# Performance work log

Hardware: AMD Instinct MI355X
Metric: run time of the kernel (lower is better)

Reference implementation:

```python
import jax, jax.numpy as jnp
import numpy as np

EPS = 1e-5  # nn.LayerNorm default

def _conv1x1(x, W):
    # x: (B,C,H,W), W: (O,C) -> (B,O,H,W)
    return jnp.einsum('bchw,oc->bohw', x, W)

def setup_inputs() -> dict:
    key = jax.random.key(0)
    kx, k1, k2, k3, k4, k5 = jax.random.split(key, 6)
    B, C, H, W = 16, 512, 64, 64
    inner = C // 2
    s = 1.0 / np.sqrt(C)
    return {
        'x':   jax.random.normal(kx, (B, C, H, W), dtype=jnp.float32),
        'Wsq': jax.random.normal(k1, (inner, C), dtype=jnp.float32) * s,
        'Wsv': jax.random.normal(k2, (inner, C), dtype=jnp.float32) * s,
        'Wcq': jax.random.normal(k3, (1, C), dtype=jnp.float32) * s,
        'Wcv': jax.random.normal(k4, (inner, C), dtype=jnp.float32) * s,
        'Wcz': jax.random.normal(k5, (C, inner), dtype=jnp.float32) * (1.0 / np.sqrt(inner)),
        'gamma': jnp.ones((C,), dtype=jnp.float32),
        'beta':  jnp.zeros((C,), dtype=jnp.float32),
    }

def _channel_pool(x, Wcq, Wcv, Wcz, gamma, beta):
    B, C, H, W = x.shape
    HW = H * W
    # channel_q: 1x1 conv to 1 channel -> (B, HW), softmax over HW
    cm = jnp.einsum('bchw,c->bhw', x, Wcq[0]).reshape(B, HW)
    cm = jax.nn.softmax(cm, axis=-1)                      # (B, HW)
    # channel_v: (B, inner, HW)
    iv = _conv1x1(x, Wcv).reshape(B, Wcv.shape[0], HW)
    context = jnp.einsum('bkn,bn->bk', iv, cm)            # (B, inner)
    z = jnp.einsum('bk,ok->bo', context, Wcz)             # (B, out)
    mu = jnp.mean(z, axis=-1, keepdims=True)
    var = jnp.mean((z - mu) ** 2, axis=-1, keepdims=True)
    zn = (z - mu) * jax.lax.rsqrt(var + EPS) * gamma + beta
    mask = jax.nn.sigmoid(zn)[:, :, None, None]           # (B, out, 1, 1)
    return x * mask

def _spatial_pool(x, Wsq, Wsv):
    B, C, H, W = x.shape
    HW = H * W
    g = _conv1x1(x, Wsq)                                  # (B, inner, H, W)
    avg = jnp.mean(g, axis=(2, 3))                        # (B, inner)
    avg = jax.nn.softmax(avg, axis=-1)                    # softmax over inner channels
    theta = _conv1x1(x, Wsv).reshape(B, Wsv.shape[0], HW) # (B, inner, HW)
    ctx = jnp.einsum('bk,bkn->bn', avg, theta).reshape(B, 1, H, W)
    return x * jax.nn.sigmoid(ctx)

def reference(x, Wsq, Wsv, Wcq, Wcv, Wcz, gamma, beta):
    # layout='parallel'
    ch = _channel_pool(x, Wcq, Wcv, Wcz, gamma, beta)
    sp = _spatial_pool(x, Wsq, Wsv)
    return ch + sp
```

## Files before the change

kernel.cpp:

```cpp
#include <hip/hip_runtime.h>
#include <math.h>

#define BB 16
#define CC 512
#define HWN 4096
#define INNER 256
#define EPSV 1e-5f

__device__ __forceinline__ float wave_sum(float s) {
    for (int off = 32; off; off >>= 1) s += __shfl_down(s, off);
    return s;
}
__device__ __forceinline__ float block_sum(float v, volatile float* s_red) {
    for (int off = 32; off; off >>= 1) v += __shfl_down(v, off);
    __syncthreads();
    if ((threadIdx.x & 63) == 0) s_red[threadIdx.x >> 6] = v;
    __syncthreads();
    return s_red[0] + s_red[1] + s_red[2] + s_red[3];
}
__device__ __forceinline__ float block_max(float v, volatile float* s_red) {
    for (int off = 32; off; off >>= 1) v = fmaxf(v, __shfl_down(v, off));
    __syncthreads();
    if ((threadIdx.x & 63) == 0) s_red[threadIdx.x >> 6] = v;
    __syncthreads();
    return fmaxf(fmaxf(s_red[0], s_red[1]), fmaxf(s_red[2], s_red[3]));
}
__device__ __forceinline__ float fsigmoid(float v) {
    return __builtin_amdgcn_rcpf(1.f + __expf(-v));
}

__global__ __launch_bounds__(256) void kA(
    const float* __restrict__ x, const float* __restrict__ wcq,
    float* __restrict__ cm_part, float* __restrict__ xsum_part)
{
    const int t = threadIdx.x, lane = t & 63, w = t >> 6;
    const int hw0 = blockIdx.x * 256;
    const int q   = blockIdx.y;
    const int c0  = q * 128;
    const int b   = blockIdx.z;
    __shared__ float s_w[128];
    __shared__ float s_cm[4][256];
    if (t < 128) s_w[t] = wcq[c0 + t];
    __syncthreads();
    const float* xb = x + ((size_t)b * CC + c0) * HWN + hw0 + lane * 4;
    float* xsp = xsum_part + ((size_t)b * 16 + blockIdx.x) * CC + c0;
    float4 acc = {0.f, 0.f, 0.f, 0.f};
    #pragma unroll 8
    for (int ci = 0; ci < 32; ++ci) {
        const int cl = w + ci * 4;
        float4 v = *(const float4*)(xb + (size_t)cl * HWN);
        const float wc = s_w[cl];
        acc.x = fmaf(v.x, wc, acc.x); acc.y = fmaf(v.y, wc, acc.y);
        acc.z = fmaf(v.z, wc, acc.z); acc.w = fmaf(v.w, wc, acc.w);
        float s = (v.x + v.y) + (v.z + v.w);
        s = wave_sum(s);
        if (lane == 0) xsp[cl] = s;
    }
    *(float4*)&s_cm[w][lane * 4] = acc;
    __syncthreads();
    cm_part[((size_t)b * 4 + q) * HWN + hw0 + t] =
        (s_cm[0][t] + s_cm[1][t]) + (s_cm[2][t] + s_cm[3][t]);
}

__global__ __launch_bounds__(256) void k2a_cmstats(
    const float* __restrict__ cm_part, float* __restrict__ cmstats)
{
    const int b = blockIdx.x, t = threadIdx.x;
    __shared__ float s_red[4];
    const float* p0 = cm_part + (size_t)b * 4 * HWN;
    const float* p1 = p0 + HWN;
    const float* p2 = p1 + HWN;
    const float* p3 = p2 + HWN;
    float lmax = -1e30f;
    #pragma unroll 4
    for (int i = t; i < HWN; i += 256)
        lmax = fmaxf(lmax, (p0[i] + p1[i]) + (p2[i] + p3[i]));
    lmax = block_max(lmax, s_red);
    float lsum = 0.f;
    #pragma unroll 4
    for (int i = t; i < HWN; i += 256)
        lsum += __expf((p0[i] + p1[i]) + (p2[i] + p3[i]) - lmax);
    lsum = block_sum(lsum, s_red);
    if (t == 0) {
        cmstats[2 * b]     = lmax;
        cmstats[2 * b + 1] = __builtin_amdgcn_rcpf(lsum);
    }
}

__global__ __launch_bounds__(256) void k_mvp(
    const float* __restrict__ W, const float* __restrict__ vpart,
    float* __restrict__ y, float scale)
{
    const int b = blockIdx.x, t = threadIdx.x, lane = t & 63, w = t >> 6;
    const int k0 = blockIdx.y * 64;
    __shared__ float s_v[CC];
    const float* xp = vpart + (size_t)b * 16 * CC;
    float a0 = 0.f, a1 = 0.f;
    #pragma unroll
    for (int blk = 0; blk < 16; ++blk) {
        a0 += xp[blk * CC + t];
        a1 += xp[blk * CC + t + 256];
    }
    s_v[t] = a0; s_v[t + 256] = a1;
    __syncthreads();
    float4 x0 = *(const float4*)&s_v[lane * 4];
    float4 x1 = *(const float4*)&s_v[256 + lane * 4];
    #pragma unroll 8
    for (int i = 0; i < 16; ++i) {
        const int k = k0 + w * 16 + i;
        const float* row = W + (size_t)k * CC + lane * 4;
        float4 q0 = *(const float4*)(row);
        float4 q1 = *(const float4*)(row + 256);
        float s = fmaf(q0.x,x0.x, fmaf(q0.y,x0.y, fmaf(q0.z,x0.z, q0.w*x0.w)))
                + fmaf(q1.x,x1.x, fmaf(q1.y,x1.y, fmaf(q1.z,x1.z, q1.w*x1.w)));
        s = wave_sum(s);
        if (lane == 0) y[b * INNER + k] = s * scale;
    }
}

__global__ __launch_bounds__(256) void k2c_wsv(
    const float* __restrict__ Wsv, const float* __restrict__ avg_logits,
    float* __restrict__ wsv_eff)
{
    const int b = blockIdx.x, t = threadIdx.x;
    const int c = blockIdx.y * 256 + t;
    __shared__ float s_red[4];
    __shared__ float s_sm[INNER];
    float a = avg_logits[b * INNER + t];
    float m = block_max(a, s_red);
    float e = __expf(a - m);
    float s2 = block_sum(e, s_red);
    s_sm[t] = e * __builtin_amdgcn_rcpf(s2);
    __syncthreads();
    float acc = 0.f;
    #pragma unroll 8
    for (int k = 0; k < INNER; ++k)
        acc = fmaf(s_sm[k], Wsv[(size_t)k * CC + c], acc);
    wsv_eff[b * CC + c] = acc;
}

__global__ __launch_bounds__(256) void kC(
    const float* __restrict__ x, const float* __restrict__ wsv_eff,
    const float* __restrict__ cm_part, const float* __restrict__ cmstats,
    float* __restrict__ ctx_part, float* __restrict__ xw_part)
{
    const int t = threadIdx.x, lane = t & 63, w = t >> 6;
    const int hw0 = blockIdx.x * 256;
    const int q   = blockIdx.y;
    const int c0  = q * 128;
    const int b   = blockIdx.z;
    __shared__ float s_w[128];
    __shared__ float s_m[256];
    __shared__ float s_cm[4][256];
    if (t < 128) s_w[t] = wsv_eff[b * CC + c0 + t];
    const float cmax = cmstats[2 * b], crinv = cmstats[2 * b + 1];
    const size_t cb = (size_t)b * 4 * HWN + hw0 + t;
    const float cmv = (cm_part[cb] + cm_part[cb + HWN])
                    + (cm_part[cb + 2 * HWN] + cm_part[cb + 3 * HWN]);
    s_m[t] = __expf(cmv - cmax) * crinv;
    __syncthreads();
    float4 mreg = *(const float4*)&s_m[lane * 4];
    const float* xb = x + ((size_t)b * CC + c0) * HWN + hw0 + lane * 4;
    float* xwp = xw_part + ((size_t)b * 16 + blockIdx.x) * CC + c0;
    float4 acc = {0.f, 0.f, 0.f, 0.f};
    #pragma unroll 8
    for (int ci = 0; ci < 32; ++ci) {
        const int cl = w + ci * 4;
        float4 v = *(const float4*)(xb + (size_t)cl * HWN);
        const float wc = s_w[cl];
        acc.x = fmaf(v.x, wc, acc.x); acc.y = fmaf(v.y, wc, acc.y);
        acc.z = fmaf(v.z, wc, acc.z); acc.w = fmaf(v.w, wc, acc.w);
        float s = fmaf(v.x,mreg.x, fmaf(v.y,mreg.y, fmaf(v.z,mreg.z, v.w*mreg.w)));
        s = wave_sum(s);
        if (lane == 0) xwp[cl] = s;
    }
    *(float4*)&s_cm[w][lane * 4] = acc;
    __syncthreads();
    ctx_part[((size_t)b * 4 + q) * HWN + hw0 + t] =
        (s_cm[0][t] + s_cm[1][t]) + (s_cm[2][t] + s_cm[3][t]);
}

__global__ __launch_bounds__(256) void k4b_z(
    const float* __restrict__ Wcz, const float* __restrict__ context,
    float* __restrict__ zbuf)
{
    const int b = blockIdx.x, t = threadIdx.x, lane = t & 63, w = t >> 6;
    const int o0 = blockIdx.y * 128;
    __shared__ float s_c[INNER];
    if (t < INNER) s_c[t] = context[b * INNER + t];
    __syncthreads();
    float4 cv = *(const float4*)&s_c[lane * 4];
    #pragma unroll 8
    for (int i = 0; i < 32; ++i) {
        const int o = o0 + w * 32 + i;
        float4 qv = *(const float4*)(Wcz + (size_t)o * INNER + lane * 4);
        float s = fmaf(qv.x,cv.x, fmaf(qv.y,cv.y, fmaf(qv.z,cv.z, qv.w*cv.w)));
        s = wave_sum(s);
        if (lane == 0) zbuf[b * CC + o] = s;
    }
}

__global__ __launch_bounds__(256) void k4c_ln(
    const float* __restrict__ gamma, const float* __restrict__ beta,
    const float* __restrict__ zbuf, float* __restrict__ maskbuf)
{
    const int b = blockIdx.x, t = threadIdx.x;
    __shared__ float s_red[4];
    float z0 = zbuf[b * CC + t], z1 = zbuf[b * CC + t + 256];
    float mu = block_sum(z0 + z1, s_red) * (1.f / CC);
    float d0 = z0 - mu, d1 = z1 - mu;
    float var = block_sum(d0 * d0 + d1 * d1, s_red) * (1.f / CC);
    float rstd = rsqrtf(var + EPSV);
    maskbuf[b * CC + t]       = fsigmoid(fmaf(d0 * rstd, gamma[t],       beta[t]));
    maskbuf[b * CC + t + 256] = fsigmoid(fmaf(d1 * rstd, gamma[t + 256], beta[t + 256]));
}

__global__ __launch_bounds__(256) void kE(
    const float* __restrict__ x, const float* __restrict__ ctx_part,
    const float* __restrict__ maskbuf, float* __restrict__ out)
{
    const int t  = threadIdx.x;
    const int hw = blockIdx.x * 1024 + t * 4;
    const int c0 = blockIdx.y * 16;
    const int b  = blockIdx.z;
    const size_t pb = (size_t)b * 4 * HWN + hw;
    float4 p0 = *(const float4*)(ctx_part + pb);
    float4 p1 = *(const float4*)(ctx_part + pb + HWN);
    float4 p2 = *(const float4*)(ctx_part + pb + 2 * HWN);
    float4 p3 = *(const float4*)(ctx_part + pb + 3 * HWN);
    float4 sg;
    sg.x = fsigmoid((p0.x + p1.x) + (p2.x + p3.x));
    sg.y = fsigmoid((p0.y + p1.y) + (p2.y + p3.y));
    sg.z = fsigmoid((p0.z + p1.z) + (p2.z + p3.z));
    sg.w = fsigmoid((p0.w + p1.w) + (p2.w + p3.w));
    const float* mb = maskbuf + b * CC + c0;
    const size_t base = ((size_t)b * CC + c0) * HWN + hw;
    #pragma unroll 4
    for (int ci = 0; ci < 16; ++ci) {
        const float m = mb[ci];
        float4 xv = *(const float4*)(x + base + (size_t)ci * HWN);
        float4 o;
        o.x = xv.x * (m + sg.x);
        o.y = xv.y * (m + sg.y);
        o.z = xv.z * (m + sg.z);
        o.w = xv.w * (m + sg.w);
        *(float4*)(out + base + (size_t)ci * HWN) = o;
    }
}

extern "C" void kernel_launch(void* const* d_in, const int* in_sizes, int n_in,
                              void* d_out, int out_size, void* d_ws, size_t ws_size,
                              hipStream_t stream) {
    const float* x     = (const float*)d_in[0];
    const float* Wsq   = (const float*)d_in[1];
    const float* Wsv   = (const float*)d_in[2];
    const float* Wcq   = (const float*)d_in[3];
    const float* Wcv   = (const float*)d_in[4];
    const float* Wcz   = (const float*)d_in[5];
    const float* gamma = (const float*)d_in[6];
    const float* beta  = (const float*)d_in[7];
    float* out = (float*)d_out;
    float* ws  = (float*)d_ws;

    float* cm_part    = ws;
    float* xsum_part  = ws + 262144;
    float* ctx_part   = ws + 393216;
    float* cmstats    = ws + 655360;
    float* wsv_eff    = ws + 655392;
    float* avg_logits = ws + 663584;
    float* context    = ws + 667680;
    float* zbuf       = ws + 671776;
    float* maskbuf    = ws + 679968;

    kA<<<dim3(16, 4, BB), 256, 0, stream>>>(x, Wcq, cm_part, xsum_part);
    k2a_cmstats<<<BB, 256, 0, stream>>>(cm_part, cmstats);
    k_mvp<<<dim3(BB, 4), 256, 0, stream>>>(Wsq, xsum_part, avg_logits, 1.0f / HWN);
    k2c_wsv<<<dim3(BB, 2), 256, 0, stream>>>(Wsv, avg_logits, wsv_eff);
    kC<<<dim3(16, 4, BB), 256, 0, stream>>>(x, wsv_eff, cm_part, cmstats, ctx_part, xsum_part);
    k_mvp<<<dim3(BB, 4), 256, 0, stream>>>(Wcv, xsum_part, context, 1.0f);
    k4b_z<<<dim3(BB, 4), 256, 0, stream>>>(Wcz, context, zbuf);
    k4c_ln<<<BB, 256, 0, stream>>>(gamma, beta, zbuf, maskbuf);
    kE<<<dim3(4, 32, BB), 256, 0, stream>>>(x, ctx_part, maskbuf, out);
}
```

Before: 381.4 us.

## Widen HW tiles in streaming passes, use LDS partial reductions, fuse small kernels

The two x-streaming kernels (kA, kC) now process 512 spatial positions per block with two float4 loads per thread, halving the grid. Per-channel sums go to a shared-memory tile and are reduced afterward instead of a wave shuffle reduction per channel. The softmax-stats and Wsq matvec kernels are merged into one launch via a blockIdx.y branch, and the Wcz matvec plus LayerNorm/sigmoid are fused into one 512-thread kernel, cutting the launch count from nine to seven. The trade-off is fewer blocks for latency hiding, more LDS per block (about 43 KB), and a serial 256-long dot product per thread in kD2.

```diff
diff --git a/kernel.cpp b/kernel.cpp
--- a/kernel.cpp
+++ b/kernel.cpp
@@ -25,6 +25,14 @@
     __syncthreads();
     return fmaxf(fmaxf(s_red[0], s_red[1]), fmaxf(s_red[2], s_red[3]));
 }
+__device__ __forceinline__ float block_sum8(float v, volatile float* s_red) {
+    for (int off = 32; off; off >>= 1) v += __shfl_down(v, off);
+    __syncthreads();
+    if ((threadIdx.x & 63) == 0) s_red[threadIdx.x >> 6] = v;
+    __syncthreads();
+    return ((s_red[0] + s_red[1]) + (s_red[2] + s_red[3]))
+         + ((s_red[4] + s_red[5]) + (s_red[6] + s_red[7]));
+}
 __device__ __forceinline__ float fsigmoid(float v) {
     return __builtin_amdgcn_rcpf(1.f + __expf(-v));
 }
@@ -34,87 +42,100 @@
     float* __restrict__ cm_part, float* __restrict__ xsum_part)
 {
     const int t = threadIdx.x, lane = t & 63, w = t >> 6;
-    const int hw0 = blockIdx.x * 256;
+    const int hw0 = blockIdx.x * 512;
     const int q   = blockIdx.y;
     const int c0  = q * 128;
     const int b   = blockIdx.z;
     __shared__ float s_w[128];
-    __shared__ float s_cm[4][256];
+    __shared__ float s_cm[4][512];
+    __shared__ float s_part[4][32][65];
     if (t < 128) s_w[t] = wcq[c0 + t];
     __syncthreads();
-    const float* xb = x + ((size_t)b * CC + c0) * HWN + hw0 + lane * 4;
-    float* xsp = xsum_part + ((size_t)b * 16 + blockIdx.x) * CC + c0;
-    float4 acc = {0.f, 0.f, 0.f, 0.f};
-    #pragma unroll 8
+    const float* xb = x + ((size_t)b * CC + c0) * HWN + hw0 + lane * 8;
+    float4 a0 = {0,0,0,0}, a1 = a0;
+    #pragma unroll 4
     for (int ci = 0; ci < 32; ++ci) {
         const int cl = w + ci * 4;
-        float4 v = *(const float4*)(xb + (size_t)cl * HWN);
+        const float* p = xb + (size_t)cl * HWN;
+        float4 v0 = *(const float4*)(p);
+        float4 v1 = *(const float4*)(p + 4);
         const float wc = s_w[cl];
-        acc.x = fmaf(v.x, wc, acc.x); acc.y = fmaf(v.y, wc, acc.y);
-        acc.z = fmaf(v.z, wc, acc.z); acc.w = fmaf(v.w, wc, acc.w);
-        float s = (v.x + v.y) + (v.z + v.w);
-        s = wave_sum(s);
-        if (lane == 0) xsp[cl] = s;
-    }
-    *(float4*)&s_cm[w][lane * 4] = acc;
-    __syncthreads();
-    cm_part[((size_t)b * 4 + q) * HWN + hw0 + t] =
-        (s_cm[0][t] + s_cm[1][t]) + (s_cm[2][t] + s_cm[3][t]);
-}
-
-__global__ __launch_bounds__(256) void k2a_cmstats(
-    const float* __restrict__ cm_part, float* __restrict__ cmstats)
-{
-    const int b = blockIdx.x, t = threadIdx.x;
+        a0.x = fmaf(v0.x, wc, a0.x); a0.y = fmaf(v0.y, wc, a0.y);
+        a0.z = fmaf(v0.z, wc, a0.z); a0.w = fmaf(v0.w, wc, a0.w);
+        a1.x = fmaf(v1.x, wc, a1.x); a1.y = fmaf(v1.y, wc, a1.y);
+        a1.z = fmaf(v1.z, wc, a1.z); a1.w = fmaf(v1.w, wc, a1.w);
+        s_part[w][ci][lane] = ((v0.x + v0.y) + (v0.z + v0.w))
+                            + ((v1.x + v1.y) + (v1.z + v1.w));
+    }
+    {
+        const int r = lane & 31;
+        const int j0 = (lane >> 5) * 32;
+        float xs = 0.f;
+        #pragma unroll
+        for (int j = 0; j < 32; ++j) xs += s_part[w][r][j0 + j];
+        xs += __shfl_down(xs, 32);
+        if (lane < 32)
+            xsum_part[((size_t)b * 8 + blockIdx.x) * CC + c0 + w + r * 4] = xs;
+    }
+    *(float4*)&s_cm[w][lane * 8]     = a0;
+    *(float4*)&s_cm[w][lane * 8 + 4] = a1;
+    __syncthreads();
+    float* cp = cm_part + ((size_t)b * 4 + q) * HWN + hw0;
+    cp[t]       = (s_cm[0][t]       + s_cm[1][t])       + (s_cm[2][t]       + s_cm[3][t]);
+    cp[t + 256] = (s_cm[0][t + 256] + s_cm[1][t + 256]) + (s_cm[2][t + 256] + s_cm[3][t + 256]);
+}
+
+__global__ __launch_bounds__(256) void kB1(
+    const float* __restrict__ Wsq, const float* __restrict__ cm_part,
+    const float* __restrict__ xsum_part,
+    float* __restrict__ cmstats, float* __restrict__ avg_logits)
+{
+    const int b = blockIdx.x, t = threadIdx.x, lane = t & 63, w = t >> 6;
     __shared__ float s_red[4];
-    const float* p0 = cm_part + (size_t)b * 4 * HWN;
-    const float* p1 = p0 + HWN;
-    const float* p2 = p1 + HWN;
-    const float* p3 = p2 + HWN;
-    float lmax = -1e30f;
-    #pragma unroll 4
-    for (int i = t; i < HWN; i += 256)
-        lmax = fmaxf(lmax, (p0[i] + p1[i]) + (p2[i] + p3[i]));
-    lmax = block_max(lmax, s_red);
-    float lsum = 0.f;
-    #pragma unroll 4
-    for (int i = t; i < HWN; i += 256)
-        lsum += __expf((p0[i] + p1[i]) + (p2[i] + p3[i]) - lmax);
-    lsum = block_sum(lsum, s_red);
-    if (t == 0) {
-        cmstats[2 * b]     = lmax;
-        cmstats[2 * b + 1] = __builtin_amdgcn_rcpf(lsum);
-    }
-}
-
-__global__ __launch_bounds__(256) void k_mvp(
-    const float* __restrict__ W, const float* __restrict__ vpart,
-    float* __restrict__ y, float scale)
-{
-    const int b = blockIdx.x, t = threadIdx.x, lane = t & 63, w = t >> 6;
-    const int k0 = blockIdx.y * 64;
     __shared__ float s_v[CC];
-    const float* xp = vpart + (size_t)b * 16 * CC;
-    float a0 = 0.f, a1 = 0.f;
-    #pragma unroll
-    for (int blk = 0; blk < 16; ++blk) {
-        a0 += xp[blk * CC + t];
-        a1 += xp[blk * CC + t + 256];
-    }
-    s_v[t] = a0; s_v[t + 256] = a1;
-    __syncthreads();
-    float4 x0 = *(const float4*)&s_v[lane * 4];
-    float4 x1 = *(const float4*)&s_v[256 + lane * 4];
-    #pragma unroll 8
-    for (int i = 0; i < 16; ++i) {
-        const int k = k0 + w * 16 + i;
-        const float* row = W + (size_t)k * CC + lane * 4;
-        float4 q0 = *(const float4*)(row);
-        float4 q1 = *(const float4*)(row + 256);
-        float s = fmaf(q0.x,x0.x, fmaf(q0.y,x0.y, fmaf(q0.z,x0.z, q0.w*x0.w)))
-                + fmaf(q1.x,x1.x, fmaf(q1.y,x1.y, fmaf(q1.z,x1.z, q1.w*x1.w)));
-        s = wave_sum(s);
-        if (lane == 0) y[b * INNER + k] = s * scale;
+    if (blockIdx.y == 4) {
+        const float* p0 = cm_part + (size_t)b * 4 * HWN;
+        const float* p1 = p0 + HWN;
+        const float* p2 = p1 + HWN;
+        const float* p3 = p2 + HWN;
+        float lmax = -1e30f;
+        #pragma unroll 4
+        for (int i = t; i < HWN; i += 256)
+            lmax = fmaxf(lmax, (p0[i] + p1[i]) + (p2[i] + p3[i]));
+        lmax = block_max(lmax, s_red);
+        float lsum = 0.f;
+        #pragma unroll 4
+        for (int i = t; i < HWN; i += 256)
+            lsum += __expf((p0[i] + p1[i]) + (p2[i] + p3[i]) - lmax);
+        lsum = block_sum(lsum, s_red);
+        if (t == 0) {
+            cmstats[2 * b]     = lmax;
+            cmstats[2 * b + 1] = __builtin_amdgcn_rcpf(lsum);
+        }
+    } else {
+        const int k0 = blockIdx.y * 64;
+        const float* xp = xsum_part + (size_t)b * 8 * CC;
+        float a0 = 0.f, a1 = 0.f;
+        #pragma unroll
+        for (int blk = 0; blk < 8; ++blk) {
+            a0 += xp[blk * CC + t];
+            a1 += xp[blk * CC + t + 256];
+        }
+        s_v[t] = a0; s_v[t + 256] = a1;
+        __syncthreads();
+        float4 x0 = *(const float4*)&s_v[lane * 4];
+        float4 x1 = *(const float4*)&s_v[256 + lane * 4];
+        #pragma unroll 8
+        for (int i = 0; i < 16; ++i) {
+            const int k = k0 + w * 16 + i;
+            const float* row = Wsq + (size_t)k * CC + lane * 4;
+            float4 q0 = *(const float4*)(row);
+            float4 q1 = *(const float4*)(row + 256);
+            float s = fmaf(q0.x,x0.x, fmaf(q0.y,x0.y, fmaf(q0.z,x0.z, q0.w*x0.w)))
+                    + fmaf(q1.x,x1.x, fmaf(q1.y,x1.y, fmaf(q1.z,x1.z, q1.w*x1.w)));
+            s = wave_sum(s);
+            if (lane == 0) avg_logits[b * INNER + k] = s * (1.0f / HWN);
+        }
     }
 }
 
@@ -145,74 +166,113 @@
     float* __restrict__ ctx_part, float* __restrict__ xw_part)
 {
     const int t = threadIdx.x, lane = t & 63, w = t >> 6;
-    const int hw0 = blockIdx.x * 256;
+    const int hw0 = blockIdx.x * 512;
     const int q   = blockIdx.y;
     const int c0  = q * 128;
     const int b   = blockIdx.z;
     __shared__ float s_w[128];
-    __shared__ float s_m[256];
-    __shared__ float s_cm[4][256];
+    __shared__ float s_m[512];
+    __shared__ float s_cm[4][512];
+    __shared__ float s_part[4][32][65];
     if (t < 128) s_w[t] = wsv_eff[b * CC + c0 + t];
     const float cmax = cmstats[2 * b], crinv = cmstats[2 * b + 1];
-    const size_t cb = (size_t)b * 4 * HWN + hw0 + t;
-    const float cmv = (cm_part[cb] + cm_part[cb + HWN])
-                    + (cm_part[cb + 2 * HWN] + cm_part[cb + 3 * HWN]);
-    s_m[t] = __expf(cmv - cmax) * crinv;
-    __syncthreads();
-    float4 mreg = *(const float4*)&s_m[lane * 4];
-    const float* xb = x + ((size_t)b * CC + c0) * HWN + hw0 + lane * 4;
-    float* xwp = xw_part + ((size_t)b * 16 + blockIdx.x) * CC + c0;
-    float4 acc = {0.f, 0.f, 0.f, 0.f};
-    #pragma unroll 8
+    {
+        const size_t cb = (size_t)b * 4 * HWN + hw0;
+        float cmv0 = (cm_part[cb + t]           + cm_part[cb + HWN + t])
+                   + (cm_part[cb + 2*HWN + t]   + cm_part[cb + 3*HWN + t]);
+        float cmv1 = (cm_part[cb + t+256]         + cm_part[cb + HWN + t+256])
+                   + (cm_part[cb + 2*HWN + t+256] + cm_part[cb + 3*HWN + t+256]);
+        s_m[t]       = __expf(cmv0 - cmax) * crinv;
+        s_m[t + 256] = __expf(cmv1 - cmax) * crinv;
+    }
+    __syncthreads();
+    float4 m0 = *(const float4*)&s_m[lane * 8];
+    float4 m1 = *(const float4*)&s_m[lane * 8 + 4];
+    const float* xb = x + ((size_t)b * CC + c0) * HWN + hw0 + lane * 8;
+    float4 a0 = {0,0,0,0}, a1 = a0;
+    #pragma unroll 4
     for (int ci = 0; ci < 32; ++ci) {
         const int cl = w + ci * 4;
-        float4 v = *(const float4*)(xb + (size_t)cl * HWN);
+        const float* p = xb + (size_t)cl * HWN;
+        float4 v0 = *(const float4*)(p);
+        float4 v1 = *(const float4*)(p + 4);
         const float wc = s_w[cl];
-        acc.x = fmaf(v.x, wc, acc.x); acc.y = fmaf(v.y, wc, acc.y);
-        acc.z = fmaf(v.z, wc, acc.z); acc.w = fmaf(v.w, wc, acc.w);
-        float s = fmaf(v.x,mreg.x, fmaf(v.y,mreg.y, fmaf(v.z,mreg.z, v.w*mreg.w)));
+        a0.x = fmaf(v0.x, wc, a0.x); a0.y = fmaf(v0.y, wc, a0.y);
+        a0.z = fmaf(v0.z, wc, a0.z); a0.w = fmaf(v0.w, wc, a0.w);
+        a1.x = fmaf(v1.x, wc, a1.x); a1.y = fmaf(v1.y, wc, a1.y);
+        a1.z = fmaf(v1.z, wc, a1.z); a1.w = fmaf(v1.w, wc, a1.w);
+        s_part[w][ci][lane] =
+              fmaf(v0.x,m0.x, fmaf(v0.y,m0.y, fmaf(v0.z,m0.z, v0.w*m0.w)))
+            + fmaf(v1.x,m1.x, fmaf(v1.y,m1.y, fmaf(v1.z,m1.z, v1.w*m1.w)));
+    }
+    {
+        const int r = lane & 31;
+        const int j0 = (lane >> 5) * 32;
+        float xs = 0.f;
+        #pragma unroll
+        for (int j = 0; j < 32; ++j) xs += s_part[w][r][j0 + j];
+        xs += __shfl_down(xs, 32);
+        if (lane < 32)
+            xw_part[((size_t)b * 8 + blockIdx.x) * CC + c0 + w + r * 4] = xs;
+    }
+    *(float4*)&s_cm[w][lane * 8]     = a0;
+    *(float4*)&s_cm[w][lane * 8 + 4] = a1;
+    __syncthreads();
+    float* cp = ctx_part + ((size_t)b * 4 + q) * HWN + hw0;
+    cp[t]       = (s_cm[0][t]       + s_cm[1][t])       + (s_cm[2][t]       + s_cm[3][t]);
+    cp[t + 256] = (s_cm[0][t + 256] + s_cm[1][t + 256]) + (s_cm[2][t + 256] + s_cm[3][t + 256]);
+}
+
+__global__ __launch_bounds__(256) void kD1(
+    const float* __restrict__ Wcv, const float* __restrict__ xw_part,
+    float* __restrict__ context)
+{
+    const int b = blockIdx.x, t = threadIdx.x, lane = t & 63, w = t >> 6;
+    const int k0 = blockIdx.y * 64;
+    __shared__ float s_v[CC];
+    const float* xp = xw_part + (size_t)b * 8 * CC;
+    float a0 = 0.f, a1 = 0.f;
+    #pragma unroll
+    for (int blk = 0; blk < 8; ++blk) {
+        a0 += xp[blk * CC + t];
+        a1 += xp[blk * CC + t + 256];
+    }
+    s_v[t] = a0; s_v[t + 256] = a1;
+    __syncthreads();
+    float4 x0 = *(const float4*)&s_v[lane * 4];
+    float4 x1 = *(const float4*)&s_v[256 + lane * 4];
+    #pragma unroll 8
+    for (int i = 0; i < 16; ++i) {
+        const int k = k0 + w * 16 + i;
+        const float* row = Wcv + (size_t)k * CC + lane * 4;
+        float4 q0 = *(const float4*)(row);
+        float4 q1 = *(const float4*)(row + 256);
+        float s = fmaf(q0.x,x0.x, fmaf(q0.y,x0.y, fmaf(q0.z,x0.z, q0.w*x0.w)))
+                + fmaf(q1.x,x1.x, fmaf(q1.y,x1.y, fmaf(q1.z,x1.z, q1.w*x1.w)));
         s = wave_sum(s);
-        if (lane == 0) xwp[cl] = s;
-    }
-    *(float4*)&s_cm[w][lane * 4] = acc;
-    __syncthreads();
-    ctx_part[((size_t)b * 4 + q) * HWN + hw0 + t] =
-        (s_cm[0][t] + s_cm[1][t]) + (s_cm[2][t] + s_cm[3][t]);
-}
-
-__global__ __launch_bounds__(256) void k4b_z(
+        if (lane == 0) context[b * INNER + k] = s;
+    }
+}
+
+__global__ __launch_bounds__(512) void kD2(
     const float* __restrict__ Wcz, const float* __restrict__ context,
-    float* __restrict__ zbuf)
-{
-    const int b = blockIdx.x, t = threadIdx.x, lane = t & 63, w = t >> 6;
-    const int o0 = blockIdx.y * 128;
+    const float* __restrict__ gamma, const float* __restrict__ beta,
+    float* __restrict__ maskbuf)
+{
+    const int b = blockIdx.x, t = threadIdx.x;
+    __shared__ float s_red[8];
     __shared__ float s_c[INNER];
     if (t < INNER) s_c[t] = context[b * INNER + t];
     __syncthreads();
-    float4 cv = *(const float4*)&s_c[lane * 4];
+    float acc = 0.f;
+    const float* wr = Wcz + (size_t)t * INNER;
     #pragma unroll 8
-    for (int i = 0; i < 32; ++i) {
-        const int o = o0 + w * 32 + i;
-        float4 qv = *(const float4*)(Wcz + (size_t)o * INNER + lane * 4);
-        float s = fmaf(qv.x,cv.x, fmaf(qv.y,cv.y, fmaf(qv.z,cv.z, qv.w*cv.w)));
-        s = wave_sum(s);
-        if (lane == 0) zbuf[b * CC + o] = s;
-    }
-}
-
-__global__ __launch_bounds__(256) void k4c_ln(
-    const float* __restrict__ gamma, const float* __restrict__ beta,
-    const float* __restrict__ zbuf, float* __restrict__ maskbuf)
-{
-    const int b = blockIdx.x, t = threadIdx.x;
-    __shared__ float s_red[4];
-    float z0 = zbuf[b * CC + t], z1 = zbuf[b * CC + t + 256];
-    float mu = block_sum(z0 + z1, s_red) * (1.f / CC);
-    float d0 = z0 - mu, d1 = z1 - mu;
-    float var = block_sum(d0 * d0 + d1 * d1, s_red) * (1.f / CC);
+    for (int k = 0; k < INNER; ++k) acc = fmaf(wr[k], s_c[k], acc);
+    float mu = block_sum8(acc, s_red) * (1.f / CC);
+    float d = acc - mu;
+    float var = block_sum8(d * d, s_red) * (1.f / CC);
     float rstd = rsqrtf(var + EPSV);
-    maskbuf[b * CC + t]       = fsigmoid(fmaf(d0 * rstd, gamma[t],       beta[t]));
-    maskbuf[b * CC + t + 256] = fsigmoid(fmaf(d1 * rstd, gamma[t + 256], beta[t + 256]));
+    maskbuf[b * CC + t] = fsigmoid(fmaf(d * rstd, gamma[t], beta[t]));
 }
 
 __global__ __launch_bounds__(256) void kE(
@@ -264,21 +324,18 @@
 
     float* cm_part    = ws;
     float* xsum_part  = ws + 262144;
-    float* ctx_part   = ws + 393216;
-    float* cmstats    = ws + 655360;
-    float* wsv_eff    = ws + 655392;
-    float* avg_logits = ws + 663584;
-    float* context    = ws + 667680;
-    float* zbuf       = ws + 671776;
-    float* maskbuf    = ws + 679968;
-
-    kA<<<dim3(16, 4, BB), 256, 0, stream>>>(x, Wcq, cm_part, xsum_part);
-    k2a_cmstats<<<BB, 256, 0, stream>>>(cm_part, cmstats);
-    k_mvp<<<dim3(BB, 4), 256, 0, stream>>>(Wsq, xsum_part, avg_logits, 1.0f / HWN);
+    float* ctx_part   = ws + 327680;
+    float* cmstats    = ws + 589824;
+    float* wsv_eff    = ws + 589856;
+    float* avg_logits = ws + 598048;
+    float* context    = ws + 602144;
+    float* maskbuf    = ws + 606240;
+
+    kA<<<dim3(8, 4, BB), 256, 0, stream>>>(x, Wcq, cm_part, xsum_part);
+    kB1<<<dim3(BB, 5), 256, 0, stream>>>(Wsq, cm_part, xsum_part, cmstats, avg_logits);
     k2c_wsv<<<dim3(BB, 2), 256, 0, stream>>>(Wsv, avg_logits, wsv_eff);
-    kC<<<dim3(16, 4, BB), 256, 0, stream>>>(x, wsv_eff, cm_part, cmstats, ctx_part, xsum_part);
-    k_mvp<<<dim3(BB, 4), 256, 0, stream>>>(Wcv, xsum_part, context, 1.0f);
-    k4b_z<<<dim3(BB, 4), 256, 0, stream>>>(Wcz, context, zbuf);
-    k4c_ln<<<BB, 256, 0, stream>>>(gamma, beta, zbuf, maskbuf);
+    kC<<<dim3(8, 4, BB), 256, 0, stream>>>(x, wsv_eff, cm_part, cmstats, ctx_part, xsum_part);
+    kD1<<<dim3(BB, 4), 256, 0, stream>>>(Wcv, xsum_part, context);
+    kD2<<<BB, 512, 0, stream>>>(Wcz, context, gamma, beta, maskbuf);
     kE<<<dim3(4, 32, BB), 256, 0, stream>>>(x, ctx_part, maskbuf, out);
 }
```

Measured after the change: 359.8 us. 5.7% less time.

## Fuse small GEMV/softmax/LN kernels and replace per-channel wave reductions with LDS transposes

Applied to the files above, without the earlier changes.

Merges the cmstats, Wsq matvec, softmax and Wsv projection into one kernel. It also merges the Wcv matvec, Wcz matvec, LayerNorm and the spatial sigmoid precompute into another, cutting the launch count from nine to five. In the x-streaming kernels, the per-iteration 64-lane shuffle reductions are replaced by writes to a padded LDS buffer, followed by one transposed reduction pass. The trade-off is fewer launches and less shuffle work against per-thread serial dot products over weight rows with strided, uncoalesced global reads, low-parallelism fused blocks, and extra LDS that may reduce occupancy.

```diff
diff --git a/kernel.cpp b/kernel.cpp
--- a/kernel.cpp
+++ b/kernel.cpp
@@ -24,6 +24,14 @@
     if ((threadIdx.x & 63) == 0) s_red[threadIdx.x >> 6] = v;
     __syncthreads();
     return fmaxf(fmaxf(s_red[0], s_red[1]), fmaxf(s_red[2], s_red[3]));
+}
+__device__ __forceinline__ float block_sum8(float v, volatile float* s_red) {
+    for (int off = 32; off; off >>= 1) v += __shfl_down(v, off);
+    __syncthreads();
+    if ((threadIdx.x & 63) == 0) s_red[threadIdx.x >> 6] = v;
+    __syncthreads();
+    return ((s_red[0] + s_red[1]) + (s_red[2] + s_red[3]))
+         + ((s_red[4] + s_red[5]) + (s_red[6] + s_red[7]));
 }
 __device__ __forceinline__ float fsigmoid(float v) {
     return __builtin_amdgcn_rcpf(1.f + __expf(-v));
@@ -40,11 +48,11 @@
     const int b   = blockIdx.z;
     __shared__ float s_w[128];
     __shared__ float s_cm[4][256];
+    __shared__ float s_part[4][32][65];
     if (t < 128) s_w[t] = wcq[c0 + t];
     __syncthreads();
     const float* xb = x + ((size_t)b * CC + c0) * HWN + hw0 + lane * 4;
-    float* xsp = xsum_part + ((size_t)b * 16 + blockIdx.x) * CC + c0;
-    float4 acc = {0.f, 0.f, 0.f, 0.f};
+    float4 acc = {0,0,0,0};
     #pragma unroll 8
     for (int ci = 0; ci < 32; ++ci) {
         const int cl = w + ci * 4;
@@ -52,9 +60,17 @@
         const float wc = s_w[cl];
         acc.x = fmaf(v.x, wc, acc.x); acc.y = fmaf(v.y, wc, acc.y);
         acc.z = fmaf(v.z, wc, acc.z); acc.w = fmaf(v.w, wc, acc.w);
-        float s = (v.x + v.y) + (v.z + v.w);
-        s = wave_sum(s);
-        if (lane == 0) xsp[cl] = s;
+        s_part[w][ci][lane] = (v.x + v.y) + (v.z + v.w);
+    }
+    {
+        const int r  = lane & 31;
+        const int j0 = (lane >> 5) * 32;
+        float xs = 0.f;
+        #pragma unroll
+        for (int j = 0; j < 32; ++j) xs += s_part[w][r][j0 + j];
+        xs += __shfl_down(xs, 32);
+        if (lane < 32)
+            xsum_part[((size_t)b * 16 + blockIdx.x) * CC + c0 + w + r * 4] = xs;
     }
     *(float4*)&s_cm[w][lane * 4] = acc;
     __syncthreads();
@@ -62,81 +78,68 @@
         (s_cm[0][t] + s_cm[1][t]) + (s_cm[2][t] + s_cm[3][t]);
 }
 
-__global__ __launch_bounds__(256) void k2a_cmstats(
-    const float* __restrict__ cm_part, float* __restrict__ cmstats)
+__global__ __launch_bounds__(256) void kBf(
+    const float* __restrict__ Wsq, const float* __restrict__ Wsv,
+    const float* __restrict__ cm_part, const float* __restrict__ xsum_part,
+    float* __restrict__ cmstats, float* __restrict__ wsv_eff)
 {
     const int b = blockIdx.x, t = threadIdx.x;
     __shared__ float s_red[4];
-    const float* p0 = cm_part + (size_t)b * 4 * HWN;
-    const float* p1 = p0 + HWN;
-    const float* p2 = p1 + HWN;
-    const float* p3 = p2 + HWN;
-    float lmax = -1e30f;
-    #pragma unroll 4
-    for (int i = t; i < HWN; i += 256)
-        lmax = fmaxf(lmax, (p0[i] + p1[i]) + (p2[i] + p3[i]));
-    lmax = block_max(lmax, s_red);
-    float lsum = 0.f;
-    #pragma unroll 4
-    for (int i = t; i < HWN; i += 256)
-        lsum += __expf((p0[i] + p1[i]) + (p2[i] + p3[i]) - lmax);
-    lsum = block_sum(lsum, s_red);
-    if (t == 0) {
-        cmstats[2 * b]     = lmax;
-        cmstats[2 * b + 1] = __builtin_amdgcn_rcpf(lsum);
-    }
-}
-
-__global__ __launch_bounds__(256) void k_mvp(
-    const float* __restrict__ W, const float* __restrict__ vpart,
-    float* __restrict__ y, float scale)
-{
-    const int b = blockIdx.x, t = threadIdx.x, lane = t & 63, w = t >> 6;
-    const int k0 = blockIdx.y * 64;
+    if (blockIdx.y == 2) {
+        const float* p0 = cm_part + (size_t)b * 4 * HWN;
+        const float* p1 = p0 + HWN;
+        const float* p2 = p1 + HWN;
+        const float* p3 = p2 + HWN;
+        float lmax = -1e30f;
+        #pragma unroll 4
+        for (int i = t; i < HWN; i += 256)
+            lmax = fmaxf(lmax, (p0[i] + p1[i]) + (p2[i] + p3[i]));
+        lmax = block_max(lmax, s_red);
+        float lsum = 0.f;
+        #pragma unroll 4
+        for (int i = t; i < HWN; i += 256)
+            lsum += __expf((p0[i] + p1[i]) + (p2[i] + p3[i]) - lmax);
+        lsum = block_sum(lsum, s_red);
+        if (t == 0) {
+            cmstats[2 * b]     = lmax;
+            cmstats[2 * b + 1] = __builtin_amdgcn_rcpf(lsum);
+        }
+        return;
+    }
     __shared__ float s_v[CC];
-    const float* xp = vpart + (size_t)b * 16 * CC;
-    float a0 = 0.f, a1 = 0.f;
-    #pragma unroll
-    for (int blk = 0; blk < 16; ++blk) {
-        a0 += xp[blk * CC + t];
-        a1 += xp[blk * CC + t + 256];
-    }
-    s_v[t] = a0; s_v[t + 256] = a1;
-    __syncthreads();
-    float4 x0 = *(const float4*)&s_v[lane * 4];
-    float4 x1 = *(const float4*)&s_v[256 + lane * 4];
-    #pragma unroll 8
-    for (int i = 0; i < 16; ++i) {
-        const int k = k0 + w * 16 + i;
-        const float* row = W + (size_t)k * CC + lane * 4;
-        float4 q0 = *(const float4*)(row);
-        float4 q1 = *(const float4*)(row + 256);
-        float s = fmaf(q0.x,x0.x, fmaf(q0.y,x0.y, fmaf(q0.z,x0.z, q0.w*x0.w)))
-                + fmaf(q1.x,x1.x, fmaf(q1.y,x1.y, fmaf(q1.z,x1.z, q1.w*x1.w)));
-        s = wave_sum(s);
-        if (lane == 0) y[b * INNER + k] = s * scale;
-    }
-}
-
-__global__ __launch_bounds__(256) void k2c_wsv(
-    const float* __restrict__ Wsv, const float* __restrict__ avg_logits,
-    float* __restrict__ wsv_eff)
-{
-    const int b = blockIdx.x, t = threadIdx.x;
-    const int c = blockIdx.y * 256 + t;
-    __shared__ float s_red[4];
     __shared__ float s_sm[INNER];
-    float a = avg_logits[b * INNER + t];
+    {
+        const float* xp = xsum_part + (size_t)b * 16 * CC;
+        float a0 = 0.f, a1 = 0.f;
+        #pragma unroll
+        for (int blk = 0; blk < 16; ++blk) {
+            a0 += xp[blk * CC + t];
+            a1 += xp[blk * CC + t + 256];
+        }
+        s_v[t] = a0; s_v[t + 256] = a1;
+    }
+    __syncthreads();
+    float a;
+    {
+        const float* wr = Wsq + (size_t)t * CC;
+        float d = 0.f;
+        #pragma unroll 8
+        for (int k = 0; k < CC; ++k) d = fmaf(wr[k], s_v[k], d);
+        a = d * (1.0f / HWN);
+    }
     float m = block_max(a, s_red);
     float e = __expf(a - m);
     float s2 = block_sum(e, s_red);
     s_sm[t] = e * __builtin_amdgcn_rcpf(s2);
     __syncthreads();
-    float acc = 0.f;
-    #pragma unroll 8
-    for (int k = 0; k < INNER; ++k)
-        acc = fmaf(s_sm[k], Wsv[(size_t)k * CC + c], acc);
-    wsv_eff[b * CC + c] = acc;
+    {
+        const int c = blockIdx.y * 256 + t;
+        float acc = 0.f;
+        #pragma unroll 8
+        for (int k = 0; k < INNER; ++k)
+            acc = fmaf(s_sm[k], Wsv[(size_t)k * CC + c], acc);
+        wsv_eff[b * CC + c] = acc;
+    }
 }
 
 __global__ __launch_bounds__(256) void kC(
@@ -152,17 +155,19 @@
     __shared__ float s_w[128];
     __shared__ float s_m[256];
     __shared__ float s_cm[4][256];
+    __shared__ float s_part[4][32][65];
     if (t < 128) s_w[t] = wsv_eff[b * CC + c0 + t];
-    const float cmax = cmstats[2 * b], crinv = cmstats[2 * b + 1];
-    const size_t cb = (size_t)b * 4 * HWN + hw0 + t;
-    const float cmv = (cm_part[cb] + cm_part[cb + HWN])
-                    + (cm_part[cb + 2 * HWN] + cm_part[cb + 3 * HWN]);
-    s_m[t] = __expf(cmv - cmax) * crinv;
+    {
+        const float cmax = cmstats[2 * b], crinv = cmstats[2 * b + 1];
+        const size_t cb = (size_t)b * 4 * HWN + hw0 + t;
+        const float cmv = (cm_part[cb] + cm_part[cb + HWN])
+                        + (cm_part[cb + 2 * HWN] + cm_part[cb + 3 * HWN]);
+        s_m[t] = __expf(cmv - cmax) * crinv;
+    }
     __syncthreads();
     float4 mreg = *(const float4*)&s_m[lane * 4];
     const float* xb = x + ((size_t)b * CC + c0) * HWN + hw0 + lane * 4;
-    float* xwp = xw_part + ((size_t)b * 16 + blockIdx.x) * CC + c0;
-    float4 acc = {0.f, 0.f, 0.f, 0.f};
+    float4 acc = {0,0,0,0};
     #pragma unroll 8
     for (int ci = 0; ci < 32; ++ci) {
         const int cl = w + ci * 4;
@@ -170,9 +175,18 @@
         const float wc = s_w[cl];
         acc.x = fmaf(v.x, wc, acc.x); acc.y = fmaf(v.y, wc, acc.y);
         acc.z = fmaf(v.z, wc, acc.z); acc.w = fmaf(v.w, wc, acc.w);
-        float s = fmaf(v.x,mreg.x, fmaf(v.y,mreg.y, fmaf(v.z,mreg.z, v.w*mreg.w)));
-        s = wave_sum(s);
-        if (lane == 0) xwp[cl] = s;
+        s_part[w][ci][lane] =
+            fmaf(v.x,mreg.x, fmaf(v.y,mreg.y, fmaf(v.z,mreg.z, v.w*mreg.w)));
+    }
+    {
+        const int r  = lane & 31;
+        const int j0 = (lane >> 5) * 32;
+        float xs = 0.f;
+        #pragma unroll
+        for (int j = 0; j < 32; ++j) xs += s_part[w][r][j0 + j];
+        xs += __shfl_down(xs, 32);
+        if (lane < 32)
+            xw_part[((size_t)b * 16 + blockIdx.x) * CC + c0 + w + r * 4] = xs;
     }
     *(float4*)&s_cm[w][lane * 4] = acc;
     __syncthreads();
@@ -180,59 +194,69 @@
         (s_cm[0][t] + s_cm[1][t]) + (s_cm[2][t] + s_cm[3][t]);
 }
 
-__global__ __launch_bounds__(256) void k4b_z(
-    const float* __restrict__ Wcz, const float* __restrict__ context,
-    float* __restrict__ zbuf)
-{
-    const int b = blockIdx.x, t = threadIdx.x, lane = t & 63, w = t >> 6;
-    const int o0 = blockIdx.y * 128;
-    __shared__ float s_c[INNER];
-    if (t < INNER) s_c[t] = context[b * INNER + t];
-    __syncthreads();
-    float4 cv = *(const float4*)&s_c[lane * 4];
-    #pragma unroll 8
-    for (int i = 0; i < 32; ++i) {
-        const int o = o0 + w * 32 + i;
-        float4 qv = *(const float4*)(Wcz + (size_t)o * INNER + lane * 4);
-        float s = fmaf(qv.x,cv.x, fmaf(qv.y,cv.y, fmaf(qv.z,cv.z, qv.w*cv.w)));
-        s = wave_sum(s);
-        if (lane == 0) zbuf[b * CC + o] = s;
-    }
-}
-
-__global__ __launch_bounds__(256) void k4c_ln(
+__global__ __launch_bounds__(512) void kDf(
+    const float* __restrict__ Wcv, const float* __restrict__ Wcz,
     const float* __restrict__ gamma, const float* __restrict__ beta,
-    const float* __restrict__ zbuf, float* __restrict__ maskbuf)
+    const float* __restrict__ ctx_part, const float* __restrict__ xw_part,
+    float* __restrict__ ctxsig, float* __restrict__ maskbuf)
 {
     const int b = blockIdx.x, t = threadIdx.x;
-    __shared__ float s_red[4];
-    float z0 = zbuf[b * CC + t], z1 = zbuf[b * CC + t + 256];
-    float mu = block_sum(z0 + z1, s_red) * (1.f / CC);
-    float d0 = z0 - mu, d1 = z1 - mu;
-    float var = block_sum(d0 * d0 + d1 * d1, s_red) * (1.f / CC);
+    if (blockIdx.y < 4) {
+        const int hw = blockIdx.y * 1024 + t * 2;
+        const size_t pb = (size_t)b * 4 * HWN + hw;
+        float2 p0 = *(const float2*)(ctx_part + pb);
+        float2 p1 = *(const float2*)(ctx_part + pb + HWN);
+        float2 p2 = *(const float2*)(ctx_part + pb + 2 * HWN);
+        float2 p3 = *(const float2*)(ctx_part + pb + 3 * HWN);
+        float2 sg;
+        sg.x = fsigmoid((p0.x + p1.x) + (p2.x + p3.x));
+        sg.y = fsigmoid((p0.y + p1.y) + (p2.y + p3.y));
+        *(float2*)(ctxsig + (size_t)b * HWN + hw) = sg;
+        return;
+    }
+    __shared__ float s_red[8];
+    __shared__ float s_v[CC];
+    __shared__ float s_ctx[INNER];
+    {
+        const float* xp = xw_part + (size_t)b * 16 * CC;
+        float a0 = 0.f;
+        #pragma unroll
+        for (int blk = 0; blk < 16; ++blk) a0 += xp[blk * CC + t];
+        s_v[t] = a0;
+    }
+    __syncthreads();
+    if (t < INNER) {
+        const float* wr = Wcv + (size_t)t * CC;
+        float d = 0.f;
+        #pragma unroll 8
+        for (int k = 0; k < CC; ++k) d = fmaf(wr[k], s_v[k], d);
+        s_ctx[t] = d;
+    }
+    __syncthreads();
+    float z;
+    {
+        const float* wr = Wcz + (size_t)t * INNER;
+        float d = 0.f;
+        #pragma unroll 8
+        for (int k = 0; k < INNER; ++k) d = fmaf(wr[k], s_ctx[k], d);
+        z = d;
+    }
+    float mu = block_sum8(z, s_red) * (1.f / CC);
+    float d = z - mu;
+    float var = block_sum8(d * d, s_red) * (1.f / CC);
     float rstd = rsqrtf(var + EPSV);
-    maskbuf[b * CC + t]       = fsigmoid(fmaf(d0 * rstd, gamma[t],       beta[t]));
-    maskbuf[b * CC + t + 256] = fsigmoid(fmaf(d1 * rstd, gamma[t + 256], beta[t + 256]));
+    maskbuf[b * CC + t] = fsigmoid(fmaf(d * rstd, gamma[t], beta[t]));
 }
 
 __global__ __launch_bounds__(256) void kE(
-    const float* __restrict__ x, const float* __restrict__ ctx_part,
+    const float* __restrict__ x, const float* __restrict__ ctxsig,
     const float* __restrict__ maskbuf, float* __restrict__ out)
 {
     const int t  = threadIdx.x;
     const int hw = blockIdx.x * 1024 + t * 4;
     const int c0 = blockIdx.y * 16;
     const int b  = blockIdx.z;
-    const size_t pb = (size_t)b * 4 * HWN + hw;
-    float4 p0 = *(const float4*)(ctx_part + pb);
-    float4 p1 = *(const float4*)(ctx_part + pb + HWN);
-    float4 p2 = *(const float4*)(ctx_part + pb + 2 * HWN);
-    float4 p3 = *(const float4*)(ctx_part + pb + 3 * HWN);
-    float4 sg;
-    sg.x = fsigmoid((p0.x + p1.x) + (p2.x + p3.x));
-    sg.y = fsigmoid((p0.y + p1.y) + (p2.y + p3.y));
-    sg.z = fsigmoid((p0.z + p1.z) + (p2.z + p3.z));
-    sg.w = fsigmoid((p0.w + p1.w) + (p2.w + p3.w));
+    float4 sg = *(const float4*)(ctxsig + (size_t)b * HWN + hw);
     const float* mb = maskbuf + b * CC + c0;
     const size_t base = ((size_t)b * CC + c0) * HWN + hw;
     #pragma unroll 4
@@ -262,23 +286,17 @@
     float* out = (float*)d_out;
     float* ws  = (float*)d_ws;
 
-    float* cm_part    = ws;
-    float* xsum_part  = ws + 262144;
-    float* ctx_part   = ws + 393216;
-    float* cmstats    = ws + 655360;
-    float* wsv_eff    = ws + 655392;
-    float* avg_logits = ws + 663584;
-    float* context    = ws + 667680;
-    float* zbuf       = ws + 671776;
-    float* maskbuf    = ws + 679968;
+    float* cm_part   = ws;
+    float* xsum_part = ws + 262144;
+    float* ctx_part  = ws + 393216;
+    float* cmstats   = ws + 655360;
+    float* wsv_eff   = ws + 655392;
+    float* ctxsig    = ws + 663584;
+    float* maskbuf   = ws + 729120;
 
     kA<<<dim3(16, 4, BB), 256, 0, stream>>>(x, Wcq, cm_part, xsum_part);
-    k2a_cmstats<<<BB, 256, 0, stream>>>(cm_part, cmstats);
-    k_mvp<<<dim3(BB, 4), 256, 0, stream>>>(Wsq, xsum_part, avg_logits, 1.0f / HWN);
-    k2c_wsv<<<dim3(BB, 2), 256, 0, stream>>>(Wsv, avg_logits, wsv_eff);
+    kBf<<<dim3(BB, 3), 256, 0, stream>>>(Wsq, Wsv, cm_part, xsum_part, cmstats, wsv_eff);
     kC<<<dim3(16, 4, BB), 256, 0, stream>>>(x, wsv_eff, cm_part, cmstats, ctx_part, xsum_part);
-    k_mvp<<<dim3(BB, 4), 256, 0, stream>>>(Wcv, xsum_part, context, 1.0f);
-    k4b_z<<<dim3(BB, 4), 256, 0, stream>>>(Wcz, context, zbuf);
-    k4c_ln<<<BB, 256, 0, stream>>>(gamma, beta, zbuf, maskbuf);
-    kE<<<dim3(4, 32, BB), 256, 0, stream>>>(x, ctx_part, maskbuf, out);
-}
+    kDf<<<dim3(BB, 5), 512, 0, stream>>>(Wcv, Wcz, gamma, beta, ctx_part, xsum_part, ctxsig, maskbuf);
+    kE<<<dim3(4, 32, BB), 256, 0, stream>>>(x, ctxsig, maskbuf, out);
+}
```

Result: no change. 381.3 us (-0.0%).
